# Kernel tuning notes

Measured on AMD Instinct MI355X. Metric: run time of the kernel, lower is better.

## Reference

```python
import jax, jax.numpy as jnp
import numpy as np

B, C, H, W = 4, 512, 64, 64
C8 = C // 8


def setup_inputs() -> dict:
    key = jax.random.key(0)
    ks = jax.random.split(key, 12)
    s = lambda fan_in: 1.0 / np.sqrt(fan_in)
    return {
        "final_encoded": jax.random.normal(ks[0], (B, C, H, W), jnp.float32),
        "total": jax.random.normal(ks[1], (B, C, H, W), jnp.float32),
        # 1x1 conv weights (out, in) and biases
        "Wq": jax.random.normal(ks[2], (C8, C), jnp.float32) * s(C),
        "bq": jax.random.normal(ks[3], (C8,), jnp.float32) * s(C),
        "Wk": jax.random.normal(ks[4], (C8, C), jnp.float32) * s(C),
        "bk": jax.random.normal(ks[5], (C8,), jnp.float32) * s(C),
        "Wv": jax.random.normal(ks[6], (C, C), jnp.float32) * s(C),
        "bv": jax.random.normal(ks[7], (C,), jnp.float32) * s(C),
        # learned additive positional tensors
        "height_tensor": jax.random.normal(ks[8], (1, C8, H, 1), jnp.float32),
        "width_tensor": jax.random.normal(ks[9], (1, C8, 1, W), jnp.float32),
        "gamma": jnp.zeros((1,), jnp.float32),
    }


def reference(final_encoded, total, Wq, bq, Wk, bk, Wv, bv, height_tensor, width_tensor, gamma):
    b, c, h, w = final_encoded.shape
    c8 = c // 8
    hw = h * w
    # 1x1 convs as channel matmuls
    q = jnp.einsum("oc,bchw->bohw", Wq, total) + bq[None, :, None, None]
    k = jnp.einsum("oc,bchw->bohw", Wk, final_encoded) + bk[None, :, None, None]
    v = jnp.einsum("oc,bchw->bohw", Wv, final_encoded) + bv[None, :, None, None]
    pq = q.reshape(b, c8, hw).transpose(0, 2, 1)   # [B, HW, C8]
    pk = k.reshape(b, c8, hw)                      # [B, C8, HW]
    pv = v.reshape(b, c, hw)                       # [B, C, HW]
    energy = jnp.einsum("bnc,bcm->bnm", pq, pk)    # [B, HW, HW] content energy
    pos = (height_tensor + width_tensor).reshape(c8, hw)  # [C8, HW] additive positional bias basis
    energy = energy + jnp.einsum("bnc,cm->bnm", pq, pos)
    attention = jax.nn.softmax(energy, axis=-1)
    # out = bmm(value, attention^T)
    out = jnp.einsum("bcm,bnm->bcn", pv, attention).reshape(b, c, h, w)
    return gamma * out + final_encoded
```

## Files before the change

### kernel.cpp

```cpp
#include <hip/hip_runtime.h>
#include <hip/hip_bf16.h>

#define B_   4
#define C_   512
#define C8_  64
#define HW_  4096

typedef short bf16x8 __attribute__((ext_vector_type(8)));
typedef float f32x4  __attribute__((ext_vector_type(4)));

__device__ __forceinline__ unsigned short f2bf(float f) {
  union { unsigned int i; float f; } x; x.f = f;
  unsigned int r = x.i + 0x7fffu + ((x.i >> 16) & 1u);
  return (unsigned short)(r >> 16);
}

__device__ __forceinline__ unsigned int cvtpk(float lo, float hi) {
  unsigned int r;
  asm("v_cvt_pk_bf16_f32 %0, %1, %2" : "=v"(r) : "v"(lo), "v"(hi));
  return r;
}

__device__ __forceinline__ float fexp2(float x) {
  float r;
  asm("v_exp_f32 %0, %1" : "=v"(r) : "v"(x));
  return r;
}

#define MFMA(a, b, c) __builtin_amdgcn_mfma_f32_16x16x32_bf16((a), (b), (c), 0, 0, 0)

#define LOG2E 1.44269504f
#define NEG20LOG2E -28.8539008f


__global__ __launch_bounds__(256) void proj_kernel(
    const float* __restrict__ total, const float* __restrict__ fe,
    const float* __restrict__ Wq, const float* __restrict__ bq,
    const float* __restrict__ Wk, const float* __restrict__ bk,
    const float* __restrict__ Wv, const float* __restrict__ bv,
    const float* __restrict__ ht, const float* __restrict__ wt,
    unsigned short* __restrict__ Qh, unsigned short* __restrict__ Kh,
    unsigned short* __restrict__ Vn) {
  __shared__ __align__(16) unsigned short Xs[64 * 72];
  __shared__ __align__(16) unsigned short Ws[128 * 72];
  const int t = threadIdx.x;
  const int b = blockIdx.z;
  const int y = blockIdx.y;
  const int x = blockIdx.x;
  const int m0 = x * 64;
  const int lane = t & 63, w = t >> 6, ln = lane & 15, quad = lane >> 4;
  const int rc4 = t >> 4, mq = t & 15;

  if (y < 2) {
    const float* X = (y == 0) ? total : fe;
    const float* W = (y == 0) ? Wq : Wk;
    const float* bias = (y == 0) ? bq : bk;
    unsigned short* dst = (y == 0) ? Qh : Kh;

    f32x4 acc[4];
#pragma unroll
    for (int i = 0; i < 4; ++i) acc[i] = f32x4{0.f, 0.f, 0.f, 0.f};

    for (int kb = 0; kb < 8; ++kb) {
      const int c0 = kb * 64;
#pragma unroll
      for (int i = 0; i < 4; ++i) {
        int idx = t + i * 256; int o = idx >> 4, c4 = idx & 15;
        f32x4 wv = *(const f32x4*)&W[(size_t)o * C_ + c0 + c4 * 4];
        *(uint2*)&Ws[o * 72 + c4 * 4] = make_uint2(cvtpk(wv[0], wv[1]), cvtpk(wv[2], wv[3]));
      }
      {
        f32x4 xv[4];
#pragma unroll
        for (int k = 0; k < 4; ++k)
          xv[k] = *(const f32x4*)&X[((size_t)b * C_ + c0 + rc4 * 4 + k) * HW_ + m0 + mq * 4];
#pragma unroll
        for (int j = 0; j < 4; ++j)
          *(uint2*)&Xs[(mq * 4 + j) * 72 + rc4 * 4] =
              make_uint2(cvtpk(xv[0][j], xv[1][j]), cvtpk(xv[2][j], xv[3][j]));
      }
      __syncthreads();
      bf16x8 a0 = *(const bf16x8*)&Xs[(w * 16 + ln) * 72 + quad * 8];
      bf16x8 a1 = *(const bf16x8*)&Xs[(w * 16 + ln) * 72 + 32 + quad * 8];
#pragma unroll
      for (int nt = 0; nt < 4; ++nt) {
        bf16x8 b0 = *(const bf16x8*)&Ws[(nt * 16 + ln) * 72 + quad * 8];
        bf16x8 b1 = *(const bf16x8*)&Ws[(nt * 16 + ln) * 72 + 32 + quad * 8];
        acc[nt] = MFMA(a0, b0, acc[nt]);
        acc[nt] = MFMA(a1, b1, acc[nt]);
      }
      __syncthreads();
    }

    const int h = x;
#pragma unroll
    for (int nt = 0; nt < 4; ++nt) {
      const int o = nt * 16 + ln;
      const float bz = bias[o];
      const float hv = (y == 1) ? ht[o * 64 + h] : 0.0f;
#pragma unroll
      for (int r = 0; r < 4; ++r) {
        const int mloc = w * 16 + quad * 4 + r;
        float val = acc[nt][r] + bz + hv;
        if (y == 1) val += wt[o * 64 + mloc];
        if (y == 0) val *= LOG2E;
        const size_t idx = ((size_t)b * 512 + (size_t)(x * 4 + w) * 2 + (nt >> 1)) * 512
                         + ((nt & 1) * 2 + (ln >> 3)) * 128 + (quad * 4 + r) * 8 + (ln & 7);
        dst[idx] = f2bf(val);
      }
    }
  } else {
    const int o0 = (y - 2) * 128;
    f32x4 acc[2][4];
#pragma unroll
    for (int p = 0; p < 2; ++p)
#pragma unroll
      for (int i = 0; i < 4; ++i) acc[p][i] = f32x4{0.f, 0.f, 0.f, 0.f};

    for (int kb = 0; kb < 8; ++kb) {
      const int c0 = kb * 64;
#pragma unroll
      for (int i = 0; i < 8; ++i) {
        int idx = t + i * 256; int o = idx >> 4, c4 = idx & 15;
        f32x4 wv = *(const f32x4*)&Wv[(size_t)(o0 + o) * C_ + c0 + c4 * 4];
        *(uint2*)&Ws[o * 72 + c4 * 4] = make_uint2(cvtpk(wv[0], wv[1]), cvtpk(wv[2], wv[3]));
      }
      {
        f32x4 xv[4];
#pragma unroll
        for (int k = 0; k < 4; ++k)
          xv[k] = *(const f32x4*)&fe[((size_t)b * C_ + c0 + rc4 * 4 + k) * HW_ + m0 + mq * 4];
#pragma unroll
        for (int j = 0; j < 4; ++j)
          *(uint2*)&Xs[(mq * 4 + j) * 72 + rc4 * 4] =
              make_uint2(cvtpk(xv[0][j], xv[1][j]), cvtpk(xv[2][j], xv[3][j]));
      }
      __syncthreads();
      bf16x8 aW[2][2];
#pragma unroll
      for (int p = 0; p < 2; ++p) {
        aW[p][0] = *(const bf16x8*)&Ws[((w + 4 * p) * 16 + ln) * 72 + quad * 8];
        aW[p][1] = *(const bf16x8*)&Ws[((w + 4 * p) * 16 + ln) * 72 + 32 + quad * 8];
      }
#pragma unroll
      for (int nt = 0; nt < 4; ++nt) {
        bf16x8 b0 = *(const bf16x8*)&Xs[(nt * 16 + ln) * 72 + quad * 8];
        bf16x8 b1 = *(const bf16x8*)&Xs[(nt * 16 + ln) * 72 + 32 + quad * 8];
#pragma unroll
        for (int p = 0; p < 2; ++p) {
          acc[p][nt] = MFMA(aW[p][0], b0, acc[p][nt]);
          acc[p][nt] = MFMA(aW[p][1], b1, acc[p][nt]);
        }
      }
      __syncthreads();
    }

#pragma unroll
    for (int p = 0; p < 2; ++p) {
#pragma unroll
      for (int r = 0; r < 4; ++r) {
        const int cht = (o0 >> 4) + w + 4 * p;
        const float bz = bv[cht * 16 + quad * 4 + r];
#pragma unroll
        for (int nt = 0; nt < 4; ++nt) {
          const size_t idx = (((size_t)b * 32 + cht) * 128 + (size_t)x * 2 + (nt >> 1)) * 512
                           + ((nt & 1) * 2 + (ln >> 3)) * 128 + (quad * 4 + r) * 8 + (ln & 7);
          Vn[idx] = f2bf(acc[p][nt][r] + bz);
        }
      }
    }
  }
}

__global__ __launch_bounds__(512, 4) void flash_kernel(
    const unsigned short* __restrict__ Qh, const unsigned short* __restrict__ Kh,
    const unsigned short* __restrict__ Vn, const float* __restrict__ fe,
    const float* __restrict__ gamma, float* __restrict__ out) {
  __shared__ __align__(16) unsigned short Ps[2][64 * 64];
  __shared__ float Red[2][64];

  const int t = threadIdx.x;
  const int n = blockIdx.x;
  const int xcd = n & 7;
  const int b = xcd & 3;
  const int ch0 = (xcd >> 2) * 256;
  const int q0 = (n >> 3) * 64;
  const int lane = t & 63, w = t >> 6, ln = lane & 15, quad = lane >> 4;
  const int qt = w & 3;
  const int kh = w >> 2;
  const int swz = (ln & 7) << 4;

  const unsigned short* Qb = Qh + (size_t)b * 512 * 512;
  const unsigned short* Kb = Kh + (size_t)b * 512 * 512;
  const unsigned short* Vbase = Vn + ((size_t)b * 32 + (ch0 >> 4)) * (128 * 512);

  const bf16x8 aq0 = *(const bf16x8*)&Qb[((size_t)((q0 >> 4) + qt) * 2 + 0) * 512 + lane * 8];
  const bf16x8 aq1 = *(const bf16x8*)&Qb[((size_t)((q0 >> 4) + qt) * 2 + 1) * 512 + lane * 8];

  const f32x4 CINIT = {NEG20LOG2E, NEG20LOG2E, NEG20LOG2E, NEG20LOG2E};

  float Sacc = 0.f;
  f32x4 acc[2][4];
#pragma unroll
  for (int mt = 0; mt < 2; ++mt)
#pragma unroll
    for (int nt = 0; nt < 4; ++nt) acc[mt][nt] = f32x4{0.f, 0.f, 0.f, 0.f};

  bf16x8 kf[2][2];
  bf16x8 vf[2][2];

  auto loadK = [&](int it) {
#pragma unroll
    for (int nt = 0; nt < 2; ++nt)
#pragma unroll
      for (int hf = 0; hf < 2; ++hf)
        kf[nt][hf] = *(const bf16x8*)&Kb[((size_t)(it * 4 + kh * 2 + nt) * 2 + hf) * 512 + lane * 8];
  };
  auto loadV = [&](int it) {
#pragma unroll
    for (int mt = 0; mt < 2; ++mt)
#pragma unroll
      for (int kc = 0; kc < 2; ++kc)
        vf[mt][kc] = *(const bf16x8*)&Vbase[(((size_t)(w * 2 + mt)) * 128 + it * 2 + kc) * 512 + lane * 8];
  };

  const int qrow = qt * 16 + ln;

  auto writeP = [&](f32x4 e0, f32x4 e1, char* Pw) {
    const float p0 = fexp2(e0[0]), p1 = fexp2(e0[1]);
    const float p2 = fexp2(e0[2]), p3 = fexp2(e0[3]);
    Sacc += (p0 + p1) + (p2 + p3);
    *(uint2*)(Pw + ((qrow * 128 + kh * 64 + quad * 8) ^ swz)) =
        make_uint2(cvtpk(p0, p1), cvtpk(p2, p3));
    const float s0 = fexp2(e1[0]), s1 = fexp2(e1[1]);
    const float s2 = fexp2(e1[2]), s3 = fexp2(e1[3]);
    Sacc += (s0 + s1) + (s2 + s3);
    *(uint2*)(Pw + ((qrow * 128 + kh * 64 + 32 + quad * 8) ^ swz)) =
        make_uint2(cvtpk(s0, s1), cvtpk(s2, s3));
  };

  loadK(0);
  loadV(0);

  {
    f32x4 e0 = MFMA(kf[0][0], aq0, CINIT);
    e0 = MFMA(kf[0][1], aq1, e0);
    f32x4 e1 = MFMA(kf[1][0], aq0, CINIT);
    e1 = MFMA(kf[1][1], aq1, e1);
    writeP(e0, e1, (char*)Ps[0]);
  }
  loadK(1);
  asm volatile("s_waitcnt lgkmcnt(0)" ::: "memory");
  __builtin_amdgcn_s_barrier();
  asm volatile("" ::: "memory");

  for (int it = 0; it < 64; ++it) {
    char* Prd = (char*)Ps[it & 1];
    char* Pwr = (char*)Ps[(it + 1) & 1];
    bf16x8 bp0[4];
#pragma unroll
    for (int nt = 0; nt < 4; ++nt)
      bp0[nt] = *(const bf16x8*)(Prd + ((((nt * 16 + ln) * 128 + quad * 16)) ^ swz));
    if (it < 63) {
      __builtin_amdgcn_s_setprio(1);
      f32x4 e0 = MFMA(kf[0][0], aq0, CINIT);
      e0 = MFMA(kf[0][1], aq1, e0);
      f32x4 e1 = MFMA(kf[1][0], aq0, CINIT);
      e1 = MFMA(kf[1][1], aq1, e1);
      __builtin_amdgcn_s_setprio(0);
      if (it < 62) loadK(it + 2);
      writeP(e0, e1, Pwr);
    }
    __builtin_amdgcn_s_setprio(1);
#pragma unroll
    for (int mt = 0; mt < 2; ++mt)
#pragma unroll
      for (int nt = 0; nt < 4; ++nt)
        acc[mt][nt] = MFMA(vf[mt][0], bp0[nt], acc[mt][nt]);
    __builtin_amdgcn_s_setprio(0);
    bf16x8 bp1[4];
#pragma unroll
    for (int nt = 0; nt < 4; ++nt)
      bp1[nt] = *(const bf16x8*)(Prd + ((((nt * 16 + ln) * 128 + 64 + quad * 16)) ^ swz));
    __builtin_amdgcn_s_setprio(1);
#pragma unroll
    for (int mt = 0; mt < 2; ++mt)
#pragma unroll
      for (int nt = 0; nt < 4; ++nt)
        acc[mt][nt] = MFMA(vf[mt][1], bp1[nt], acc[mt][nt]);
    __builtin_amdgcn_s_setprio(0);
    if (it < 63) {
      loadV(it + 1);
      asm volatile("s_waitcnt lgkmcnt(0)" ::: "memory");
      __builtin_amdgcn_s_barrier();
      asm volatile("" ::: "memory");
    }
  }

  {
    float s = Sacc;
    s += __shfl_xor(s, 16);
    s += __shfl_xor(s, 32);
    if (quad == 0) Red[kh][qrow] = s;
  }
  __syncthreads();
  float rsv[4];
#pragma unroll
  for (int nt = 0; nt < 4; ++nt)
    rsv[nt] = 1.0f / (Red[0][nt * 16 + ln] + Red[1][nt * 16 + ln]);

  const float g = gamma[0];
#pragma unroll
  for (int mt = 0; mt < 2; ++mt) {
#pragma unroll
    for (int r = 0; r < 4; ++r) {
      const int ch = ch0 + w * 32 + mt * 16 + quad * 4 + r;
      const size_t base = ((size_t)b * C_ + ch) * HW_ + q0;
#pragma unroll
      for (int nt = 0; nt < 4; ++nt) {
        const size_t idx = base + nt * 16 + ln;
        out[idx] = g * (acc[mt][nt][r] * rsv[nt]) + fe[idx];
      }
    }
  }
}

extern "C" void kernel_launch(void* const* d_in, const int* in_sizes, int n_in,
                              void* d_out, int out_size, void* d_ws, size_t ws_size,
                              hipStream_t stream) {
  const float* fe    = (const float*)d_in[0];
  const float* total = (const float*)d_in[1];
  const float* Wq    = (const float*)d_in[2];
  const float* bq    = (const float*)d_in[3];
  const float* Wk    = (const float*)d_in[4];
  const float* bk    = (const float*)d_in[5];
  const float* Wv    = (const float*)d_in[6];
  const float* bv    = (const float*)d_in[7];
  const float* ht    = (const float*)d_in[8];
  const float* wt    = (const float*)d_in[9];
  const float* gamma = (const float*)d_in[10];
  float* out = (float*)d_out;

  unsigned short* Qh = (unsigned short*)d_ws;
  unsigned short* Kh = Qh + (size_t)B_ * HW_ * C8_;
  unsigned short* Vn = Kh + (size_t)B_ * HW_ * C8_;

  proj_kernel<<<dim3(64, 6, B_), 256, 0, stream>>>(total, fe, Wq, bq, Wk, bk,
                                                   Wv, bv, ht, wt, Qh, Kh, Vn);
  flash_kernel<<<dim3(512), 512, 0, stream>>>(Qh, Kh, Vn, fe, gamma, out);
}
```

Measured before the change: 228.2 us.

## Merge Q/K/V projections into one block per spatial tile sharing input loads

The projection kernel now launches one 640-thread block per (spatial tile, batch) that computes all 640 output channels (Q, K, V) together, instead of six separate blocks per tile. Each block stages both fe and total tiles once in shared memory, so fe is no longer re-read and re-converted by the K block and four V blocks. Each wave now computes a 64x64 output tile with more accumulators. The cost is far fewer blocks (256), larger LDS use (about 110 KB) and higher register pressure, which lowers occupancy and leaves the flash kernel unchanged.

```diff
diff --git a/kernel.cpp b/kernel.cpp
--- a/kernel.cpp
+++ b/kernel.cpp
@@ -33,7 +33,7 @@
 #define NEG20LOG2E -28.8539008f
 
 
-__global__ __launch_bounds__(256) void proj_kernel(
+__global__ __launch_bounds__(640) void proj_kernel(
     const float* __restrict__ total, const float* __restrict__ fe,
     const float* __restrict__ Wq, const float* __restrict__ bq,
     const float* __restrict__ Wk, const float* __restrict__ bk,
@@ -41,131 +41,114 @@
     const float* __restrict__ ht, const float* __restrict__ wt,
     unsigned short* __restrict__ Qh, unsigned short* __restrict__ Kh,
     unsigned short* __restrict__ Vn) {
-  __shared__ __align__(16) unsigned short Xs[64 * 72];
-  __shared__ __align__(16) unsigned short Ws[128 * 72];
+  __shared__ __align__(16) unsigned short Ws[640 * 72];
+  __shared__ __align__(16) unsigned short Xf[64 * 72];
+  __shared__ __align__(16) unsigned short Xt[64 * 72];
+
   const int t = threadIdx.x;
-  const int b = blockIdx.z;
-  const int y = blockIdx.y;
+  const int b = blockIdx.y;
   const int x = blockIdx.x;
   const int m0 = x * 64;
   const int lane = t & 63, w = t >> 6, ln = lane & 15, quad = lane >> 4;
-  const int rc4 = t >> 4, mq = t & 15;
-
-  if (y < 2) {
-    const float* X = (y == 0) ? total : fe;
-    const float* W = (y == 0) ? Wq : Wk;
-    const float* bias = (y == 0) ? bq : bk;
-    unsigned short* dst = (y == 0) ? Qh : Kh;
-
-    f32x4 acc[4];
-#pragma unroll
-    for (int i = 0; i < 4; ++i) acc[i] = f32x4{0.f, 0.f, 0.f, 0.f};
-
-    for (int kb = 0; kb < 8; ++kb) {
-      const int c0 = kb * 64;
-#pragma unroll
-      for (int i = 0; i < 4; ++i) {
-        int idx = t + i * 256; int o = idx >> 4, c4 = idx & 15;
-        f32x4 wv = *(const f32x4*)&W[(size_t)o * C_ + c0 + c4 * 4];
-        *(uint2*)&Ws[o * 72 + c4 * 4] = make_uint2(cvtpk(wv[0], wv[1]), cvtpk(wv[2], wv[3]));
+
+  const int c4 = t & 15;
+  const int orow = t >> 4;
+
+  f32x4 acc[4][4];
+#pragma unroll
+  for (int ct = 0; ct < 4; ++ct)
+#pragma unroll
+    for (int mt = 0; mt < 4; ++mt) acc[ct][mt] = f32x4{0.f, 0.f, 0.f, 0.f};
+
+  for (int kb = 0; kb < 8; ++kb) {
+    const int c0 = kb * 64;
+#pragma unroll
+    for (int i = 0; i < 16; ++i) {
+      const int o = i * 40 + orow;
+      const float* src = (o < 64) ? &Wq[(size_t)o * C_]
+                       : (o < 128) ? &Wk[(size_t)(o - 64) * C_]
+                                   : &Wv[(size_t)(o - 128) * C_];
+      f32x4 wv = *(const f32x4*)&src[c0 + c4 * 4];
+      *(uint2*)&Ws[o * 72 + c4 * 4] =
+          make_uint2(cvtpk(wv[0], wv[1]), cvtpk(wv[2], wv[3]));
+    }
+    if (t < 512) {
+      const int t2 = t & 255;
+      const float* Xsrc = (t < 256) ? fe : total;
+      unsigned short* Xdst = (t < 256) ? Xf : Xt;
+      const int rc4 = t2 >> 4, mq = t2 & 15;
+      f32x4 xv[4];
+#pragma unroll
+      for (int k = 0; k < 4; ++k)
+        xv[k] = *(const f32x4*)&Xsrc[((size_t)b * C_ + c0 + rc4 * 4 + k) * HW_ + m0 + mq * 4];
+#pragma unroll
+      for (int j = 0; j < 4; ++j)
+        *(uint2*)&Xdst[(mq * 4 + j) * 72 + rc4 * 4] =
+            make_uint2(cvtpk(xv[0][j], xv[1][j]), cvtpk(xv[2][j], xv[3][j]));
+    }
+    __syncthreads();
+    const unsigned short* Xsel = (w == 0) ? Xt : Xf;
+    bf16x8 aw[4][2], bx[4][2];
+#pragma unroll
+    for (int ct = 0; ct < 4; ++ct) {
+      aw[ct][0] = *(const bf16x8*)&Ws[(w * 64 + ct * 16 + ln) * 72 + quad * 8];
+      aw[ct][1] = *(const bf16x8*)&Ws[(w * 64 + ct * 16 + ln) * 72 + 32 + quad * 8];
+    }
+#pragma unroll
+    for (int mt = 0; mt < 4; ++mt) {
+      bx[mt][0] = *(const bf16x8*)&Xsel[(mt * 16 + ln) * 72 + quad * 8];
+      bx[mt][1] = *(const bf16x8*)&Xsel[(mt * 16 + ln) * 72 + 32 + quad * 8];
+    }
+#pragma unroll
+    for (int ct = 0; ct < 4; ++ct)
+#pragma unroll
+      for (int mt = 0; mt < 4; ++mt) {
+        acc[ct][mt] = MFMA(aw[ct][0], bx[mt][0], acc[ct][mt]);
+        acc[ct][mt] = MFMA(aw[ct][1], bx[mt][1], acc[ct][mt]);
       }
-      {
-        f32x4 xv[4];
-#pragma unroll
-        for (int k = 0; k < 4; ++k)
-          xv[k] = *(const f32x4*)&X[((size_t)b * C_ + c0 + rc4 * 4 + k) * HW_ + m0 + mq * 4];
-#pragma unroll
-        for (int j = 0; j < 4; ++j)
-          *(uint2*)&Xs[(mq * 4 + j) * 72 + rc4 * 4] =
-              make_uint2(cvtpk(xv[0][j], xv[1][j]), cvtpk(xv[2][j], xv[3][j]));
-      }
-      __syncthreads();
-      bf16x8 a0 = *(const bf16x8*)&Xs[(w * 16 + ln) * 72 + quad * 8];
-      bf16x8 a1 = *(const bf16x8*)&Xs[(w * 16 + ln) * 72 + 32 + quad * 8];
-#pragma unroll
-      for (int nt = 0; nt < 4; ++nt) {
-        bf16x8 b0 = *(const bf16x8*)&Ws[(nt * 16 + ln) * 72 + quad * 8];
-        bf16x8 b1 = *(const bf16x8*)&Ws[(nt * 16 + ln) * 72 + 32 + quad * 8];
-        acc[nt] = MFMA(a0, b0, acc[nt]);
-        acc[nt] = MFMA(a1, b1, acc[nt]);
-      }
-      __syncthreads();
-    }
-
-    const int h = x;
-#pragma unroll
-    for (int nt = 0; nt < 4; ++nt) {
-      const int o = nt * 16 + ln;
-      const float bz = bias[o];
-      const float hv = (y == 1) ? ht[o * 64 + h] : 0.0f;
+    __syncthreads();
+  }
+
+  if (w == 0) {
+#pragma unroll
+    for (int ct = 0; ct < 4; ++ct)
+#pragma unroll
+      for (int mt = 0; mt < 4; ++mt)
+#pragma unroll
+        for (int r = 0; r < 4; ++r) {
+          const int o = ct * 16 + quad * 4 + r;
+          const float val = (acc[ct][mt][r] + bq[o]) * LOG2E;
+          const size_t idx = ((size_t)b * 512 + (x * 4 + mt) * 2 + (ct >> 1)) * 512
+                           + ((((ct & 1) << 1) | (quad >> 1))) * 128
+                           + ln * 8 + ((quad & 1) << 2) + r;
+          Qh[idx] = f2bf(val);
+        }
+  } else if (w == 1) {
+#pragma unroll
+    for (int ct = 0; ct < 4; ++ct)
+#pragma unroll
+      for (int mt = 0; mt < 4; ++mt)
+#pragma unroll
+        for (int r = 0; r < 4; ++r) {
+          const int o = ct * 16 + quad * 4 + r;
+          const float val = acc[ct][mt][r] + bk[o] + ht[o * 64 + x] + wt[o * 64 + mt * 16 + ln];
+          const size_t idx = ((size_t)b * 512 + (x * 4 + mt) * 2 + (ct >> 1)) * 512
+                           + ((((ct & 1) << 1) | (quad >> 1))) * 128
+                           + ln * 8 + ((quad & 1) << 2) + r;
+          Kh[idx] = f2bf(val);
+        }
+  } else {
+#pragma unroll
+    for (int ct = 0; ct < 4; ++ct) {
+      const int cht = w * 4 - 8 + ct;
 #pragma unroll
       for (int r = 0; r < 4; ++r) {
-        const int mloc = w * 16 + quad * 4 + r;
-        float val = acc[nt][r] + bz + hv;
-        if (y == 1) val += wt[o * 64 + mloc];
-        if (y == 0) val *= LOG2E;
-        const size_t idx = ((size_t)b * 512 + (size_t)(x * 4 + w) * 2 + (nt >> 1)) * 512
-                         + ((nt & 1) * 2 + (ln >> 3)) * 128 + (quad * 4 + r) * 8 + (ln & 7);
-        dst[idx] = f2bf(val);
-      }
-    }
-  } else {
-    const int o0 = (y - 2) * 128;
-    f32x4 acc[2][4];
-#pragma unroll
-    for (int p = 0; p < 2; ++p)
-#pragma unroll
-      for (int i = 0; i < 4; ++i) acc[p][i] = f32x4{0.f, 0.f, 0.f, 0.f};
-
-    for (int kb = 0; kb < 8; ++kb) {
-      const int c0 = kb * 64;
-#pragma unroll
-      for (int i = 0; i < 8; ++i) {
-        int idx = t + i * 256; int o = idx >> 4, c4 = idx & 15;
-        f32x4 wv = *(const f32x4*)&Wv[(size_t)(o0 + o) * C_ + c0 + c4 * 4];
-        *(uint2*)&Ws[o * 72 + c4 * 4] = make_uint2(cvtpk(wv[0], wv[1]), cvtpk(wv[2], wv[3]));
-      }
-      {
-        f32x4 xv[4];
-#pragma unroll
-        for (int k = 0; k < 4; ++k)
-          xv[k] = *(const f32x4*)&fe[((size_t)b * C_ + c0 + rc4 * 4 + k) * HW_ + m0 + mq * 4];
-#pragma unroll
-        for (int j = 0; j < 4; ++j)
-          *(uint2*)&Xs[(mq * 4 + j) * 72 + rc4 * 4] =
-              make_uint2(cvtpk(xv[0][j], xv[1][j]), cvtpk(xv[2][j], xv[3][j]));
-      }
-      __syncthreads();
-      bf16x8 aW[2][2];
-#pragma unroll
-      for (int p = 0; p < 2; ++p) {
-        aW[p][0] = *(const bf16x8*)&Ws[((w + 4 * p) * 16 + ln) * 72 + quad * 8];
-        aW[p][1] = *(const bf16x8*)&Ws[((w + 4 * p) * 16 + ln) * 72 + 32 + quad * 8];
-      }
-#pragma unroll
-      for (int nt = 0; nt < 4; ++nt) {
-        bf16x8 b0 = *(const bf16x8*)&Xs[(nt * 16 + ln) * 72 + quad * 8];
-        bf16x8 b1 = *(const bf16x8*)&Xs[(nt * 16 + ln) * 72 + 32 + quad * 8];
-#pragma unroll
-        for (int p = 0; p < 2; ++p) {
-          acc[p][nt] = MFMA(aW[p][0], b0, acc[p][nt]);
-          acc[p][nt] = MFMA(aW[p][1], b1, acc[p][nt]);
-        }
-      }
-      __syncthreads();
-    }
-
-#pragma unroll
-    for (int p = 0; p < 2; ++p) {
-#pragma unroll
-      for (int r = 0; r < 4; ++r) {
-        const int cht = (o0 >> 4) + w + 4 * p;
         const float bz = bv[cht * 16 + quad * 4 + r];
 #pragma unroll
-        for (int nt = 0; nt < 4; ++nt) {
-          const size_t idx = (((size_t)b * 32 + cht) * 128 + (size_t)x * 2 + (nt >> 1)) * 512
-                           + ((nt & 1) * 2 + (ln >> 3)) * 128 + (quad * 4 + r) * 8 + (ln & 7);
-          Vn[idx] = f2bf(acc[p][nt][r] + bz);
+        for (int mt = 0; mt < 4; ++mt) {
+          const size_t idx = (((size_t)b * 32 + cht) * 128 + (size_t)x * 2 + (mt >> 1)) * 512
+                           + (((mt & 1) * 2) + (ln >> 3)) * 128 + (quad * 4 + r) * 8 + (ln & 7);
+          Vn[idx] = f2bf(acc[ct][mt][r] + bz);
         }
       }
     }
@@ -345,7 +328,7 @@
   unsigned short* Kh = Qh + (size_t)B_ * HW_ * C8_;
   unsigned short* Vn = Kh + (size_t)B_ * HW_ * C8_;
 
-  proj_kernel<<<dim3(64, 6, B_), 256, 0, stream>>>(total, fe, Wq, bq, Wk, bk,
-                                                   Wv, bv, ht, wt, Qh, Kh, Vn);
+  proj_kernel<<<dim3(64, B_), 640, 0, stream>>>(total, fe, Wq, bq, Wk, bk,
+                                                Wv, bv, ht, wt, Qh, Kh, Vn);
   flash_kernel<<<dim3(512), 512, 0, stream>>>(Qh, Kh, Vn, fe, gamma, out);
 }
```

Result: no change. 231.8 us (+1.6%).
